# Kernel tuning notes

Hardware: AMD Instinct MI355X
Metric: run time of the kernel (lower is better)

Reference implementation:

```python
import jax, jax.numpy as jnp
import numpy as np

D_K = 128

def setup_inputs() -> dict:
    key = jax.random.key(0)
    k1, k2, k3 = jax.random.split(key, 3)
    q = jax.random.normal(k1, (8192, D_K), dtype=jnp.float32)
    k = jax.random.normal(k2, (8192, D_K), dtype=jnp.float32)
    v = jax.random.normal(k3, (8192, D_K), dtype=jnp.float32)
    return {"q": q, "k": k, "v": v}

def reference(q, k, v):
    # scores: [S_q, S_k]
    scores = jnp.einsum('qd,kd->qk', q, k) / jnp.sqrt(jnp.float32(D_K))
    attn = jax.nn.softmax(scores, axis=-1)  # softmax over keys (torch default last dim)
    return jnp.einsum('qk,kd->qd', attn, v)
```

## Files before the change

### kernel.cpp

```cpp
#include <hip/hip_runtime.h>
#include <math.h>


typedef _Float16 f16x8 __attribute__((ext_vector_type(8)));
typedef float    f32x16 __attribute__((ext_vector_type(16)));

constexpr int S_LEN = 8192;
constexpr int D_K   = 128;
constexpr int NSLICE = 8;
constexpr int ITERS  = (S_LEN / NSLICE) / 32;

constexpr size_t WS_L_OFF  = 0;
constexpr size_t KV_OFF    = 262144;
constexpr size_t PART_OFF  = KV_OFF + (size_t)256 * 16384;
constexpr size_t WS_NEED   = PART_OFF + (size_t)7 * S_LEN * D_K * 4;

#define CSCALE (0.08838834764831845f * 1.44269504088896340736f)

union UH8 { _Float16 h[8]; uint4 q; f16x8 v; };
union UF4 { unsigned u[4]; uint4 q; f16x8 v; };

__device__ inline void async16(const uint4* g, uint4* l) {
  __builtin_amdgcn_global_load_lds(
      (const __attribute__((address_space(1))) unsigned int*)g,
      (__attribute__((address_space(3))) unsigned int*)l, 16, 0, 0);
}

template <bool ZOUT>
__global__ __launch_bounds__(512) void attn_prep(const float* __restrict__ K,
                                                 const float* __restrict__ V,
                                                 float* __restrict__ out,
                                                 char* __restrict__ ws) {
  const int t = blockIdx.x * 512 + threadIdx.x;
  uint4* KVg = (uint4*)(ws + KV_OFF);
  if (t < 131072) {
    int kt = t >> 9, idx = t & 511;
    int lane = idx & 63, s = idx >> 6;
    int key = kt * 32 + (lane & 31);
    int d0  = s * 16 + (lane >> 5) * 8;
    const float4* src = (const float4*)(K + (size_t)key * D_K + d0);
    float4 a = src[0], b = src[1];
    float f[8] = {a.x, a.y, a.z, a.w, b.x, b.y, b.z, b.w};
    UH8 h;
    #pragma unroll
    for (int j = 0; j < 8; ++j) h.h[j] = (_Float16)f[j];
    KVg[(size_t)kt * 1024 + idx] = h.q;
  } else if (t < 262144) {
    int g = t - 131072;
    int kt = g >> 9, idx = g & 511;
    int lane = idx & 63, c = (idx >> 6) & 3, kstep = idx >> 8;
    int d  = c * 32 + (lane & 31);
    int kb = kt * 32 + kstep * 16 + (lane >> 5) * 8;
    UH8 h;
    #pragma unroll
    for (int j = 0; j < 8; ++j) h.h[j] = (_Float16)V[(size_t)(kb + j) * D_K + d];
    KVg[(size_t)kt * 1024 + 512 + idx] = h.q;
  } else if (ZOUT && t < 327680) {
    int i = t - 262144;
    float4 z = make_float4(0.f, 0.f, 0.f, 0.f);
    float4* o4 = (float4*)out;
    #pragma unroll
    for (int j = 0; j < 4; ++j) o4[(size_t)i * 4 + j] = z;
  } else if (ZOUT && t < 330176) {
    int i = t - 327680;
    if (i < 2048) ((float4*)(ws + WS_L_OFF))[i] = make_float4(0.f, 0.f, 0.f, 0.f);
  }
}

template <bool PARTIAL>
__global__ __launch_bounds__(256, 2)
void attn_main(const float* __restrict__ Qg, float* __restrict__ out,
               char* __restrict__ ws) {
  __shared__ uint4 KV[2][1024];

  const int tid   = threadIdx.x;
  const int wave  = tid >> 6;
  const int lane  = tid & 63;
  const int lrow  = lane & 31;
  const int lhalf = lane >> 5;

  const int blk = blockIdx.x;
  const int ks  = blk & 7;
  const int qb  = blk >> 3;
  const int qw  = qb * 128 + wave * 32;

  float* ws_l = (float*)(ws + WS_L_OFF);

  f16x8 qf[8];
  {
    const int q = qw + lrow;
    #pragma unroll
    for (int s = 0; s < 8; ++s) {
      const float4* src = (const float4*)(Qg + (size_t)q * D_K + s * 16 + lhalf * 8);
      float4 a = src[0], b = src[1];
      float f[8] = {a.x, a.y, a.z, a.w, b.x, b.y, b.z, b.w};
      UH8 h;
      #pragma unroll
      for (int j = 0; j < 8; ++j) h.h[j] = (_Float16)(f[j] * CSCALE);
      qf[s] = h.v;
    }
  }

  f32x16 O0{}, O1{}, O2{}, O3{};
  float lsum = 0.f;

  const uint4* KVg = (const uint4*)(ws + KV_OFF);

  {
    const size_t base = (size_t)(ks * ITERS) * 1024;
    #pragma unroll
    for (int i = 0; i < 4; ++i)
      async16(KVg + base + i * 256 + tid, &KV[0][i * 256 + tid]);
  }

  for (int it = 0; it < ITERS; ++it) {
    const int buf = it & 1;
    __syncthreads();

    if (it + 1 < ITERS) {
      const size_t base = (size_t)(ks * ITERS + it + 1) * 1024;
      #pragma unroll
      for (int i = 0; i < 4; ++i)
        async16(KVg + base + i * 256 + tid, &KV[buf ^ 1][i * 256 + tid]);
    }

    f32x16 Sa{}, Sb{};
    #pragma unroll
    for (int s = 0; s < 4; ++s) {
      f16x8 ka = __builtin_bit_cast(f16x8, KV[buf][(2 * s    ) * 64 + lane]);
      f16x8 kb = __builtin_bit_cast(f16x8, KV[buf][(2 * s + 1) * 64 + lane]);
      Sa = __builtin_amdgcn_mfma_f32_32x32x16_f16(ka, qf[2 * s    ], Sa, 0, 0, 0);
      Sb = __builtin_amdgcn_mfma_f32_32x32x16_f16(kb, qf[2 * s + 1], Sb, 0, 0, 0);
    }

    unsigned pk[8];
    #pragma unroll
    for (int i = 0; i < 8; ++i) {
      float p0 = __builtin_amdgcn_exp2f(Sa[2 * i]     + Sb[2 * i]);
      float p1 = __builtin_amdgcn_exp2f(Sa[2 * i + 1] + Sb[2 * i + 1]);
      lsum += p0 + p1;
      pk[i] = __builtin_bit_cast(unsigned, __builtin_amdgcn_cvt_pkrtz(p0, p1));
    }

    unsigned s0 = __shfl_xor(pk[0], 32), s1 = __shfl_xor(pk[1], 32);
    unsigned s2 = __shfl_xor(pk[2], 32), s3 = __shfl_xor(pk[3], 32);
    unsigned s4 = __shfl_xor(pk[4], 32), s5 = __shfl_xor(pk[5], 32);
    unsigned s6 = __shfl_xor(pk[6], 32), s7 = __shfl_xor(pk[7], 32);
    UF4 A0, A1;
    A0.u[0] = lhalf ? s2 : pk[0];
    A0.u[1] = lhalf ? s3 : pk[1];
    A0.u[2] = lhalf ? pk[2] : s0;
    A0.u[3] = lhalf ? pk[3] : s1;
    A1.u[0] = lhalf ? s6 : pk[4];
    A1.u[1] = lhalf ? s7 : pk[5];
    A1.u[2] = lhalf ? pk[6] : s4;
    A1.u[3] = lhalf ? pk[7] : s5;

    #pragma unroll
    for (int kstep = 0; kstep < 2; ++kstep) {
      f16x8 pf = kstep ? A1.v : A0.v;
      f16x8 v0 = __builtin_bit_cast(f16x8, KV[buf][512 + kstep * 256 +   0 + lane]);
      f16x8 v1 = __builtin_bit_cast(f16x8, KV[buf][512 + kstep * 256 +  64 + lane]);
      f16x8 v2 = __builtin_bit_cast(f16x8, KV[buf][512 + kstep * 256 + 128 + lane]);
      f16x8 v3 = __builtin_bit_cast(f16x8, KV[buf][512 + kstep * 256 + 192 + lane]);
      O0 = __builtin_amdgcn_mfma_f32_32x32x16_f16(pf, v0, O0, 0, 0, 0);
      O1 = __builtin_amdgcn_mfma_f32_32x32x16_f16(pf, v1, O1, 0, 0, 0);
      O2 = __builtin_amdgcn_mfma_f32_32x32x16_f16(pf, v2, O2, 0, 0, 0);
      O3 = __builtin_amdgcn_mfma_f32_32x32x16_f16(pf, v3, O3, 0, 0, 0);
    }
  }

  lsum += __shfl_xor(lsum, 32);

  if (PARTIAL) {
    if (lhalf == 0) ws_l[ks * S_LEN + qw + lrow] = lsum;
    float* obase = (ks == 0) ? out
                 : (float*)(ws + PART_OFF) + (size_t)(ks - 1) * S_LEN * D_K;
    #pragma unroll
    for (int r = 0; r < 16; ++r) {
      int row = (r & 3) + 8 * (r >> 2) + 4 * lhalf;
      float* dst = obase + (size_t)(qw + row) * D_K + lrow;
      dst[ 0] = O0[r];
      dst[32] = O1[r];
      dst[64] = O2[r];
      dst[96] = O3[r];
    }
  } else {
    if (lhalf == 0) atomicAdd(ws_l + qw + lrow, lsum);
    #pragma unroll
    for (int r = 0; r < 16; ++r) {
      int row = (r & 3) + 8 * (r >> 2) + 4 * lhalf;
      float* dst = out + (size_t)(qw + row) * D_K + lrow;
      atomicAdd(dst +  0, O0[r]);
      atomicAdd(dst + 32, O1[r]);
      atomicAdd(dst + 64, O2[r]);
      atomicAdd(dst + 96, O3[r]);
    }
  }
}

__global__ __launch_bounds__(256) void attn_norm(float* __restrict__ out,
                                                 const float* __restrict__ lpart,
                                                 const float* __restrict__ opart,
                                                 int nparts) {
  int i = blockIdx.x * 256 + threadIdx.x;
  int q = i >> 5;
  float4* o4 = (float4*)out;
  float4 acc = o4[i];
  float l = lpart[q];
  for (int s = 1; s <= nparts; ++s) {
    float4 p = ((const float4*)opart)[(size_t)(s - 1) * 262144 + i];
    acc.x += p.x; acc.y += p.y; acc.z += p.z; acc.w += p.w;
    l += lpart[s * S_LEN + q];
  }
  float inv = 1.0f / l;
  acc.x *= inv; acc.y *= inv; acc.z *= inv; acc.w *= inv;
  o4[i] = acc;
}

extern "C" void kernel_launch(void* const* d_in, const int* in_sizes, int n_in,
                              void* d_out, int out_size, void* d_ws, size_t ws_size,
                              hipStream_t stream) {
  const float* q = (const float*)d_in[0];
  const float* k = (const float*)d_in[1];
  const float* v = (const float*)d_in[2];
  float* out = (float*)d_out;
  char* ws = (char*)d_ws;
  const bool part = (ws_size >= WS_NEED);

  if (part) {
    attn_prep<false><<<dim3(512), dim3(512), 0, stream>>>(k, v, out, ws);
    attn_main<true><<<dim3(512), dim3(256), 0, stream>>>(q, out, ws);
    attn_norm<<<dim3(1024), dim3(256), 0, stream>>>(
        out, (const float*)(ws + WS_L_OFF), (const float*)(ws + PART_OFF), 7);
  } else {
    attn_prep<true><<<dim3(645), dim3(512), 0, stream>>>(k, v, out, ws);
    attn_main<false><<<dim3(512), dim3(256), 0, stream>>>(q, out, ws);
    attn_norm<<<dim3(1024), dim3(256), 0, stream>>>(
        out, (const float*)(ws + WS_L_OFF), (const float*)(ws + PART_OFF), 0);
  }
}
```

Before: 114.3 us.

## Fuse split-K reduction and normalization into main kernel via last-block counter

Removes the separate normalization launch in the partial path. Each of the eight key-slice blocks for a query block bumps a per-query-block atomic counter after a threadfence, and the last one to arrive sums the seven partial outputs plus the row sums, then normalizes and writes the output. The prep kernel gains one block to zero the counters. This saves a kernel launch and its gap, but the reduction now runs serially in whichever block finishes last, which may leave a tail at the end of the grid.

```diff
diff --git a/kernel.cpp b/kernel.cpp
--- a/kernel.cpp
+++ b/kernel.cpp
@@ -10,10 +10,11 @@
 constexpr int NSLICE = 8;
 constexpr int ITERS  = (S_LEN / NSLICE) / 32;
 
-constexpr size_t WS_L_OFF  = 0;
-constexpr size_t KV_OFF    = 262144;
-constexpr size_t PART_OFF  = KV_OFF + (size_t)256 * 16384;
-constexpr size_t WS_NEED   = PART_OFF + (size_t)7 * S_LEN * D_K * 4;
+constexpr size_t WS_L_OFF = 0;
+constexpr size_t CNT_OFF  = 262144;
+constexpr size_t KV_OFF   = 262400;
+constexpr size_t PART_OFF = KV_OFF + (size_t)256 * 16384;
+constexpr size_t WS_NEED  = PART_OFF + (size_t)7 * S_LEN * D_K * 4;
 
 #define CSCALE (0.08838834764831845f * 1.44269504088896340736f)
 
@@ -55,14 +56,18 @@
     #pragma unroll
     for (int j = 0; j < 8; ++j) h.h[j] = (_Float16)V[(size_t)(kb + j) * D_K + d];
     KVg[(size_t)kt * 1024 + 512 + idx] = h.q;
-  } else if (ZOUT && t < 327680) {
-    int i = t - 262144;
-    float4 z = make_float4(0.f, 0.f, 0.f, 0.f);
-    float4* o4 = (float4*)out;
-    #pragma unroll
-    for (int j = 0; j < 4; ++j) o4[(size_t)i * 4 + j] = z;
-  } else if (ZOUT && t < 330176) {
-    int i = t - 327680;
+  } else if (t < 262208) {
+    ((int*)(ws + CNT_OFF))[t - 262144] = 0;
+  } else if (ZOUT && t < 327744) {
+    int i = t - 262208;
+    if (i < 65536) {
+      float4 z = make_float4(0.f, 0.f, 0.f, 0.f);
+      float4* o4 = (float4*)out;
+      #pragma unroll
+      for (int j = 0; j < 4; ++j) o4[(size_t)i * 4 + j] = z;
+    }
+  } else if (ZOUT && t < 330240) {
+    int i = t - 327744;
     if (i < 2048) ((float4*)(ws + WS_L_OFF))[i] = make_float4(0.f, 0.f, 0.f, 0.f);
   }
 }
@@ -72,6 +77,8 @@
 void attn_main(const float* __restrict__ Qg, float* __restrict__ out,
                char* __restrict__ ws) {
   __shared__ uint4 KV[2][1024];
+  __shared__ int   isLast;
+  __shared__ float linv[128];
 
   const int tid   = threadIdx.x;
   const int wave  = tid >> 6;
@@ -185,6 +192,37 @@
       dst[64] = O2[r];
       dst[96] = O3[r];
     }
+
+    __threadfence();
+    if (tid == 0) {
+      int old = atomicAdd((int*)(ws + CNT_OFF) + qb, 1);
+      isLast = (old == NSLICE - 1);
+    }
+    __syncthreads();
+    if (isLast) {
+      __threadfence();
+      if (tid < 128) {
+        float l = 0.f;
+        #pragma unroll
+        for (int s = 0; s < NSLICE; ++s) l += ws_l[s * S_LEN + qb * 128 + tid];
+        linv[tid] = 1.0f / l;
+      }
+      __syncthreads();
+      const float4* pp = (const float4*)(ws + PART_OFF);
+      float4* o4 = (float4*)out;
+      for (int i = tid; i < 4096; i += 256) {
+        size_t gi = (size_t)qb * 4096 + i;
+        float4 acc = o4[gi];
+        #pragma unroll
+        for (int s = 0; s < 7; ++s) {
+          float4 p = pp[(size_t)s * 262144 + gi];
+          acc.x += p.x; acc.y += p.y; acc.z += p.z; acc.w += p.w;
+        }
+        float inv = linv[i >> 5];
+        acc.x *= inv; acc.y *= inv; acc.z *= inv; acc.w *= inv;
+        o4[gi] = acc;
+      }
+    }
   } else {
     if (lhalf == 0) atomicAdd(ws_l + qw + lrow, lsum);
     #pragma unroll
@@ -200,22 +238,13 @@
 }
 
 __global__ __launch_bounds__(256) void attn_norm(float* __restrict__ out,
-                                                 const float* __restrict__ lpart,
-                                                 const float* __restrict__ opart,
-                                                 int nparts) {
+                                                 const float* __restrict__ ws_l) {
   int i = blockIdx.x * 256 + threadIdx.x;
-  int q = i >> 5;
   float4* o4 = (float4*)out;
-  float4 acc = o4[i];
-  float l = lpart[q];
-  for (int s = 1; s <= nparts; ++s) {
-    float4 p = ((const float4*)opart)[(size_t)(s - 1) * 262144 + i];
-    acc.x += p.x; acc.y += p.y; acc.z += p.z; acc.w += p.w;
-    l += lpart[s * S_LEN + q];
-  }
-  float inv = 1.0f / l;
-  acc.x *= inv; acc.y *= inv; acc.z *= inv; acc.w *= inv;
-  o4[i] = acc;
+  float4 o = o4[i];
+  float inv = 1.0f / ws_l[i >> 5];
+  o.x *= inv; o.y *= inv; o.z *= inv; o.w *= inv;
+  o4[i] = o;
 }
 
 extern "C" void kernel_launch(void* const* d_in, const int* in_sizes, int n_in,
@@ -229,14 +258,12 @@
   const bool part = (ws_size >= WS_NEED);
 
   if (part) {
-    attn_prep<false><<<dim3(512), dim3(512), 0, stream>>>(k, v, out, ws);
+    attn_prep<false><<<dim3(513), dim3(512), 0, stream>>>(k, v, out, ws);
     attn_main<true><<<dim3(512), dim3(256), 0, stream>>>(q, out, ws);
-    attn_norm<<<dim3(1024), dim3(256), 0, stream>>>(
-        out, (const float*)(ws + WS_L_OFF), (const float*)(ws + PART_OFF), 7);
   } else {
-    attn_prep<true><<<dim3(645), dim3(512), 0, stream>>>(k, v, out, ws);
+    attn_prep<true><<<dim3(646), dim3(512), 0, stream>>>(k, v, out, ws);
     attn_main<false><<<dim3(512), dim3(256), 0, stream>>>(q, out, ws);
     attn_norm<<<dim3(1024), dim3(256), 0, stream>>>(
-        out, (const float*)(ws + WS_L_OFF), (const float*)(ws + PART_OFF), 0);
-  }
-}
+        out, (const float*)(ws + WS_L_OFF));
+  }
+}
```

Measured after the change: 219.8 us. 1.92x slower.

## Load K/V tiles directly from global into registers, dropping LDS double buffer

Applied to the files above, without the earlier changes.

Removes the shared-memory double-buffered async copy of the prepacked K/V tiles and the per-iteration __syncthreads. Each wave now reads its K and V fragments straight from global memory (L2-resident prepacked layout) into registers, with the loop unrolled by two so loads can be issued ahead of the MFMAs. This drops block-wide barriers and LDS traffic, but all four waves of a block now fetch the same tile separately, which quadruples global/L2 reads and increases register pressure. The zero-init bound tweak is cosmetic.

```diff
diff --git a/kernel.cpp b/kernel.cpp
--- a/kernel.cpp
+++ b/kernel.cpp
@@ -10,21 +10,15 @@
 constexpr int NSLICE = 8;
 constexpr int ITERS  = (S_LEN / NSLICE) / 32;
 
-constexpr size_t WS_L_OFF  = 0;
-constexpr size_t KV_OFF    = 262144;
-constexpr size_t PART_OFF  = KV_OFF + (size_t)256 * 16384;
-constexpr size_t WS_NEED   = PART_OFF + (size_t)7 * S_LEN * D_K * 4;
+constexpr size_t WS_L_OFF = 0;
+constexpr size_t KV_OFF   = 262144;
+constexpr size_t PART_OFF = KV_OFF + (size_t)256 * 16384;
+constexpr size_t WS_NEED  = PART_OFF + (size_t)7 * S_LEN * D_K * 4;
 
 #define CSCALE (0.08838834764831845f * 1.44269504088896340736f)
 
 union UH8 { _Float16 h[8]; uint4 q; f16x8 v; };
 union UF4 { unsigned u[4]; uint4 q; f16x8 v; };
-
-__device__ inline void async16(const uint4* g, uint4* l) {
-  __builtin_amdgcn_global_load_lds(
-      (const __attribute__((address_space(1))) unsigned int*)g,
-      (__attribute__((address_space(3))) unsigned int*)l, 16, 0, 0);
-}
 
 template <bool ZOUT>
 __global__ __launch_bounds__(512) void attn_prep(const float* __restrict__ K,
@@ -61,9 +55,9 @@
     float4* o4 = (float4*)out;
     #pragma unroll
     for (int j = 0; j < 4; ++j) o4[(size_t)i * 4 + j] = z;
-  } else if (ZOUT && t < 330176) {
+  } else if (ZOUT && t < 329728) {
     int i = t - 327680;
-    if (i < 2048) ((float4*)(ws + WS_L_OFF))[i] = make_float4(0.f, 0.f, 0.f, 0.f);
+    ((float4*)(ws + WS_L_OFF))[i] = make_float4(0.f, 0.f, 0.f, 0.f);
   }
 }
 
@@ -71,8 +65,6 @@
 __global__ __launch_bounds__(256, 2)
 void attn_main(const float* __restrict__ Qg, float* __restrict__ out,
                char* __restrict__ ws) {
-  __shared__ uint4 KV[2][1024];
-
   const int tid   = threadIdx.x;
   const int wave  = tid >> 6;
   const int lane  = tid & 63;
@@ -104,31 +96,23 @@
   f32x16 O0{}, O1{}, O2{}, O3{};
   float lsum = 0.f;
 
-  const uint4* KVg = (const uint4*)(ws + KV_OFF);
-
-  {
-    const size_t base = (size_t)(ks * ITERS) * 1024;
-    #pragma unroll
-    for (int i = 0; i < 4; ++i)
-      async16(KVg + base + i * 256 + tid, &KV[0][i * 256 + tid]);
-  }
-
+  const uint4* KVs = (const uint4*)(ws + KV_OFF) + (size_t)(ks * ITERS) * 1024 + lane;
+
+  #pragma unroll 2
   for (int it = 0; it < ITERS; ++it) {
-    const int buf = it & 1;
-    __syncthreads();
-
-    if (it + 1 < ITERS) {
-      const size_t base = (size_t)(ks * ITERS + it + 1) * 1024;
-      #pragma unroll
-      for (int i = 0; i < 4; ++i)
-        async16(KVg + base + i * 256 + tid, &KV[buf ^ 1][i * 256 + tid]);
-    }
+    const uint4* tb = KVs + (size_t)it * 1024;
+
+    uint4 kr[8], vr[8];
+    #pragma unroll
+    for (int s = 0; s < 8; ++s) kr[s] = tb[s * 64];
+    #pragma unroll
+    for (int f = 0; f < 8; ++f) vr[f] = tb[512 + f * 64];
 
     f32x16 Sa{}, Sb{};
     #pragma unroll
     for (int s = 0; s < 4; ++s) {
-      f16x8 ka = __builtin_bit_cast(f16x8, KV[buf][(2 * s    ) * 64 + lane]);
-      f16x8 kb = __builtin_bit_cast(f16x8, KV[buf][(2 * s + 1) * 64 + lane]);
+      f16x8 ka = __builtin_bit_cast(f16x8, kr[2 * s]);
+      f16x8 kb = __builtin_bit_cast(f16x8, kr[2 * s + 1]);
       Sa = __builtin_amdgcn_mfma_f32_32x32x16_f16(ka, qf[2 * s    ], Sa, 0, 0, 0);
       Sb = __builtin_amdgcn_mfma_f32_32x32x16_f16(kb, qf[2 * s + 1], Sb, 0, 0, 0);
     }
@@ -159,14 +143,10 @@
     #pragma unroll
     for (int kstep = 0; kstep < 2; ++kstep) {
       f16x8 pf = kstep ? A1.v : A0.v;
-      f16x8 v0 = __builtin_bit_cast(f16x8, KV[buf][512 + kstep * 256 +   0 + lane]);
-      f16x8 v1 = __builtin_bit_cast(f16x8, KV[buf][512 + kstep * 256 +  64 + lane]);
-      f16x8 v2 = __builtin_bit_cast(f16x8, KV[buf][512 + kstep * 256 + 128 + lane]);
-      f16x8 v3 = __builtin_bit_cast(f16x8, KV[buf][512 + kstep * 256 + 192 + lane]);
-      O0 = __builtin_amdgcn_mfma_f32_32x32x16_f16(pf, v0, O0, 0, 0, 0);
-      O1 = __builtin_amdgcn_mfma_f32_32x32x16_f16(pf, v1, O1, 0, 0, 0);
-      O2 = __builtin_amdgcn_mfma_f32_32x32x16_f16(pf, v2, O2, 0, 0, 0);
-      O3 = __builtin_amdgcn_mfma_f32_32x32x16_f16(pf, v3, O3, 0, 0, 0);
+      O0 = __builtin_amdgcn_mfma_f32_32x32x16_f16(pf, __builtin_bit_cast(f16x8, vr[kstep * 4 + 0]), O0, 0, 0, 0);
+      O1 = __builtin_amdgcn_mfma_f32_32x32x16_f16(pf, __builtin_bit_cast(f16x8, vr[kstep * 4 + 1]), O1, 0, 0, 0);
+      O2 = __builtin_amdgcn_mfma_f32_32x32x16_f16(pf, __builtin_bit_cast(f16x8, vr[kstep * 4 + 2]), O2, 0, 0, 0);
+      O3 = __builtin_amdgcn_mfma_f32_32x32x16_f16(pf, __builtin_bit_cast(f16x8, vr[kstep * 4 + 3]), O3, 0, 0, 0);
     }
   }
 
@@ -226,9 +206,8 @@
   const float* v = (const float*)d_in[2];
   float* out = (float*)d_out;
   char* ws = (char*)d_ws;
-  const bool part = (ws_size >= WS_NEED);
-
-  if (part) {
+
+  if (ws_size >= WS_NEED) {
     attn_prep<false><<<dim3(512), dim3(512), 0, stream>>>(k, v, out, ws);
     attn_main<true><<<dim3(512), dim3(256), 0, stream>>>(q, out, ws);
     attn_norm<<<dim3(1024), dim3(256), 0, stream>>>(
```

New measurement: 155.5 us. 1.36x slower.
